# Kernel tuning notes

Measured on AMD Instinct MI355X. Metric: run time of the kernel, lower is better.

The kernel has to match this reference:

```python
import jax, jax.numpy as jnp
import numpy as np

B, S, D, E = 8, 2048, 1024, 8


def setup_inputs() -> dict:
    key = jax.random.key(0)
    k1, k2, k3, k4 = jax.random.split(key, 4)
    return {
        "x": jax.random.normal(k1, (B, S, D), dtype=jnp.float32),
        "routing_scores": jax.random.normal(k2, (B, E), dtype=jnp.float32),
        "expert_w": jax.random.normal(k3, (E, D, D), dtype=jnp.float32) / np.sqrt(D),
        "expert_b": jax.random.normal(k4, (E, D), dtype=jnp.float32),
        "k": 2,
    }


def reference(x, routing_scores, expert_w, expert_b, k):
    batch = routing_scores.shape[0]
    # top-k gating mask + renormalization scale (torch.topk + scatter_ equivalent)
    values, indices = jax.lax.top_k(routing_scores, k)              # (B, k)
    mask = jnp.zeros_like(routing_scores, dtype=bool)
    mask = mask.at[jnp.arange(batch)[:, None], indices].set(True)    # (B, E)
    scale = 1.0 / (values.sum(axis=1, keepdims=True) + 1e-8)         # (B, 1)
    masked_scores = scale * routing_scores * mask                    # (B, E)

    # dense per-expert transform: expert_e(x) = x @ W_e + b_e  -> (E, B, S, D)
    expert_out = jnp.einsum("bsd,edf->ebsf", x, expert_w) + expert_b[:, None, None, :]
    # weighted scatter-accumulate over experts (zero weight for inactive pairs)
    final_output = jnp.einsum("be,ebsf->bsf", masked_scores, expert_out)

    return final_output, mask.sum(axis=0)
```

## Files before the change

### kernel.cpp

```cpp
#include <hip/hip_runtime.h>

#define NB 8
#define NS 2048
#define ND 1024
#define NE 8

typedef unsigned short ushort_t;
typedef __attribute__((ext_vector_type(8))) short bf16x8;
typedef __attribute__((ext_vector_type(4))) float f32x4;

__device__ __forceinline__ unsigned short f2bf(float f) {
    union { float f; unsigned int u; } x; x.f = f;
    unsigned int u = x.u + 0x7fffu + ((x.u >> 16) & 1u);
    return (unsigned short)(u >> 16);
}

__device__ __forceinline__ void gload16(const void* g, void* l) {
    __builtin_amdgcn_global_load_lds(
        (const __attribute__((address_space(1))) unsigned int*)g,
        (__attribute__((address_space(3))) unsigned int*)l, 16, 0, 0);
}

__device__ __forceinline__ void coef_local(const float* __restrict__ scores,
                                           int b, int k, float* cf) {
    float s[NE];
#pragma unroll
    for (int e = 0; e < NE; ++e) s[e] = scores[b * NE + e];
    bool sel[NE];
#pragma unroll
    for (int e = 0; e < NE; ++e) sel[e] = false;
    float sum = 0.f;
    for (int j = 0; j < k; ++j) {
        int best = 0; float bv = -3.4e38f;
#pragma unroll
        for (int e = 0; e < NE; ++e)
            if (!sel[e] && s[e] > bv) { bv = s[e]; best = e; }
        sel[best] = true; sum += bv;
    }
    float scale = 1.f / (sum + 1e-8f);
#pragma unroll
    for (int e = 0; e < NE; ++e) cf[e] = sel[e] ? scale * s[e] : 0.f;
}

__global__ void prep_kernel(const float* __restrict__ x,
                            const float* __restrict__ scores,
                            const float* __restrict__ W,
                            const float* __restrict__ eb,
                            const int* __restrict__ kp,
                            ushort_t* __restrict__ xb,
                            ushort_t* __restrict__ wct,
                            float* __restrict__ bias,
                            float* __restrict__ counts) {
    __shared__ float tile[64][65];
    __shared__ int selS[NB][NE];
    int bid = blockIdx.x;
    int t = threadIdx.x;

    if (bid < 2048) {
        int b = bid >> 8;
        int f0 = (bid & 15) * 64, d0 = ((bid >> 4) & 15) * 64;
        float cf[NE];
        coef_local(scores, b, kp[0], cf);
        int lr = t >> 4;
        int lc = (t & 15) * 4;
        float4 acc[4];
#pragma unroll
        for (int it = 0; it < 4; ++it) acc[it] = make_float4(0.f, 0.f, 0.f, 0.f);
#pragma unroll
        for (int e = 0; e < NE; ++e) {
            float c = cf[e];
            if (c != 0.f) {
                const float* We = W + ((size_t)e * ND * ND);
#pragma unroll
                for (int it = 0; it < 4; ++it) {
                    int d = d0 + lr + it * 16;
                    float4 v = *(const float4*)(We + (size_t)d * ND + f0 + lc);
                    acc[it].x += c * v.x; acc[it].y += c * v.y;
                    acc[it].z += c * v.z; acc[it].w += c * v.w;
                }
            }
        }
#pragma unroll
        for (int it = 0; it < 4; ++it) {
            int r = lr + it * 16;
            tile[r][lc + 0] = acc[it].x; tile[r][lc + 1] = acc[it].y;
            tile[r][lc + 2] = acc[it].z; tile[r][lc + 3] = acc[it].w;
        }
        __syncthreads();
        int dl = t & 63;
        int frow = t >> 6;
        ushort_t* dst = wct + (size_t)b * ND * ND + (size_t)f0 * ND + d0 + dl;
#pragma unroll
        for (int it = 0; it < 16; ++it) {
            int f = frow + it * 4;
            dst[(size_t)f * ND] = f2bf(tile[dl][f]);
        }
    } else if (bid < 10240) {
        size_t i = (size_t)(bid - 2048) * 256 + t;
        const float4* p = (const float4*)x + 2 * i;
        float4 a = p[0], b = p[1];
        uint4 o;
        o.x = (unsigned)f2bf(a.x) | ((unsigned)f2bf(a.y) << 16);
        o.y = (unsigned)f2bf(a.z) | ((unsigned)f2bf(a.w) << 16);
        o.z = (unsigned)f2bf(b.x) | ((unsigned)f2bf(b.y) << 16);
        o.w = (unsigned)f2bf(b.z) | ((unsigned)f2bf(b.w) << 16);
        ((uint4*)xb)[i] = o;
    } else if (bid < 10272) {
        int i = bid - 10240;
        int b = i >> 2, f = (i & 3) * 256 + t;
        float cf[NE];
        coef_local(scores, b, kp[0], cf);
        float acc = 0.f;
#pragma unroll
        for (int e = 0; e < NE; ++e)
            if (cf[e] != 0.f) acc += cf[e] * eb[e * ND + f];
        bias[b * ND + f] = acc;
    } else {
        int k = kp[0];
        if (t < NB) {
            float s[NE];
#pragma unroll
            for (int e = 0; e < NE; ++e) s[e] = scores[t * NE + e];
            bool sel[NE];
#pragma unroll
            for (int e = 0; e < NE; ++e) sel[e] = false;
            for (int j = 0; j < k; ++j) {
                int best = 0; float bv = -3.4e38f;
#pragma unroll
                for (int e = 0; e < NE; ++e)
                    if (!sel[e] && s[e] > bv) { bv = s[e]; best = e; }
                sel[best] = true;
            }
#pragma unroll
            for (int e = 0; e < NE; ++e) selS[t][e] = sel[e] ? 1 : 0;
        }
        __syncthreads();
        if (t < NE) {
            int c = 0;
#pragma unroll
            for (int b = 0; b < NB; ++b) c += selS[b][t];
            counts[t] = (float)c;
        }
    }
}

__global__ __launch_bounds__(512, 2) void gemm_kernel(const ushort_t* __restrict__ xb,
                                                      const ushort_t* __restrict__ wct,
                                                      const float* __restrict__ bias,
                                                      float* __restrict__ out) {
    __shared__ ushort_t ldsA[3][256 * 32];
    __shared__ ushort_t ldsB[3][256 * 32];

    int bid = blockIdx.x;
    int b = bid & 7;
    int tile = bid >> 3;
    int m0 = (tile >> 2) * 256;
    int n0 = (tile & 3) * 256;
    const ushort_t* A  = xb  + ((size_t)b * NS * ND) + (size_t)m0 * ND;
    const ushort_t* Bt = wct + ((size_t)b * ND * ND) + (size_t)n0 * ND;

    int t = threadIdx.x, lane = t & 63, wave = t >> 6;
    int wm = wave >> 2, wn = wave & 3;
    int fr = lane & 15, fq = lane >> 4;

    int swz_s = (lane & 3) ^ ((lane >> 3) & 3);
    const ushort_t* srcA = A  + (size_t)(wave * 16 + (lane >> 2)) * ND + swz_s * 8;
    const ushort_t* srcB = Bt + (size_t)(wave * 16 + (lane >> 2)) * ND + swz_s * 8;
    int dst0 = wave * 512;
    int dst1 = (8 + wave) * 512;

    int swz_r = fq ^ ((fr >> 1) & 3);
    int offA = (wm * 128 + fr) * 32 + swz_r * 8;
    int offB = (wn * 64  + fr) * 32 + swz_r * 8;

    f32x4 acc[8][4];
#pragma unroll
    for (int i = 0; i < 8; ++i)
#pragma unroll
        for (int j = 0; j < 4; ++j) acc[i][j] = (f32x4){0.f, 0.f, 0.f, 0.f};

    const int NT = 32;

#define STAGE(kt, buf) do { \
    gload16(srcA + (kt) * 32,                     &ldsA[buf][dst0]); \
    gload16(srcA + (kt) * 32 + 128 * ND,          &ldsA[buf][dst1]); \
    gload16(srcB + (kt) * 32,                     &ldsB[buf][dst0]); \
    gload16(srcB + (kt) * 32 + 128 * ND,          &ldsB[buf][dst1]); \
} while (0)

#define READF(aR, bR, rb) do { \
    const ushort_t* pA_ = &ldsA[rb][0] + offA; \
    const ushort_t* pB_ = &ldsB[rb][0] + offB; \
    _Pragma("unroll") \
    for (int nj = 0; nj < 4; ++nj) bR[nj] = *(const bf16x8*)(pB_ + nj * 512); \
    _Pragma("unroll") \
    for (int mi = 0; mi < 8; ++mi) aR[mi] = *(const bf16x8*)(pA_ + mi * 512); \
} while (0)

#define MFMA_T(aR, bR) do { \
    __builtin_amdgcn_s_setprio(1); \
    _Pragma("unroll") \
    for (int mi = 0; mi < 8; ++mi) \
        _Pragma("unroll") \
        for (int nj = 0; nj < 4; ++nj) \
            acc[mi][nj] = __builtin_amdgcn_mfma_f32_16x16x32_bf16(aR[mi], bR[nj], acc[mi][nj], 0, 0, 0); \
    __builtin_amdgcn_s_setprio(0); \
} while (0)

#define TILE_END(j) do { \
    if ((j) + 2 < NT) { \
        asm volatile("s_waitcnt lgkmcnt(0)" ::: "memory"); \
        if ((j) + 3 < NT) asm volatile("s_waitcnt vmcnt(4)" ::: "memory"); \
        else              asm volatile("s_waitcnt vmcnt(0)" ::: "memory"); \
        __builtin_amdgcn_s_barrier(); \
    } \
} while (0)

    bf16x8 aX[8], bX[4], aY[8], bY[4];

    STAGE(0, 0); STAGE(1, 1); STAGE(2, 2);
    asm volatile("s_waitcnt vmcnt(4)" ::: "memory");
    __builtin_amdgcn_s_barrier();
    READF(aX, bX, 0);
    asm volatile("s_waitcnt lgkmcnt(0)" ::: "memory");
    __builtin_amdgcn_s_barrier();

    int cs = 0;
    for (int kt = 0; kt < NT; kt += 2) {
        int rb = cs + 1; if (rb == 3) rb = 0;
        READF(aY, bY, rb);
        if (kt + 3 < NT) STAGE(kt + 3, cs);
        __builtin_amdgcn_sched_barrier(0);
        MFMA_T(aX, bX);
        __builtin_amdgcn_sched_barrier(0);
        TILE_END(kt);

        int rb2 = rb + 1; if (rb2 == 3) rb2 = 0;
        if (kt + 2 < NT) READF(aX, bX, rb2);
        if (kt + 4 < NT) STAGE(kt + 4, rb);
        __builtin_amdgcn_sched_barrier(0);
        MFMA_T(aY, bY);
        __builtin_amdgcn_sched_barrier(0);
        TILE_END(kt + 1);

        cs = rb2;
    }

#undef STAGE
#undef READF
#undef MFMA_T
#undef TILE_END

    const float* bs = bias + b * ND;
    float* O = out + ((size_t)b * NS * ND);
#pragma unroll
    for (int mi = 0; mi < 8; ++mi) {
        int row = m0 + wm * 128 + mi * 16 + fq * 4;
#pragma unroll
        for (int nj = 0; nj < 4; ++nj) {
            int col = n0 + wn * 64 + nj * 16 + fr;
            float bv = bs[col];
            f32x4 v = acc[mi][nj];
#pragma unroll
            for (int r = 0; r < 4; ++r)
                O[(size_t)(row + r) * ND + col] = v[r] + bv;
        }
    }
}

extern "C" void kernel_launch(void* const* d_in, const int* in_sizes, int n_in,
                              void* d_out, int out_size, void* d_ws, size_t ws_size,
                              hipStream_t stream) {
    const float* x      = (const float*)d_in[0];
    const float* scores = (const float*)d_in[1];
    const float* Wx     = (const float*)d_in[2];
    const float* eb     = (const float*)d_in[3];
    const int*   kp     = (const int*)d_in[4];
    float* out = (float*)d_out;
    char* ws = (char*)d_ws;

    float*    bias  = (float*)(ws + 1024);
    ushort_t* xbuf  = (ushort_t*)(ws + 65536);
    ushort_t* wct   = (ushort_t*)(ws + 65536 + (size_t)NB * NS * ND * 2);
    float*    counts = out + (size_t)NB * NS * ND;

    prep_kernel<<<10273, 256, 0, stream>>>(x, scores, Wx, eb, kp, xbuf, wct, bias, counts);
    gemm_kernel<<<256, 512, 0, stream>>>(xbuf, wct, bias, out);
}
```

Measured before the change: 67.18 us.

## Restructure GEMM main loop into four-phase ping-pong with finer-grained staging

Replaces the triple-buffered 32-wide K pipeline with a double-buffered 64-wide K tile split into two halves. Each K step becomes four phases of 16 MFMAs, and each phase interleaves a slice of LDS fragment reads and global-to-LDS loads with a barrier gate. The LDS swizzle and per-thread staging layout also change. The aim is to lower register pressure and overlap memory traffic with MFMA work more finely, at the cost of more barriers per K step.

```diff
diff --git a/kernel.cpp b/kernel.cpp
--- a/kernel.cpp
+++ b/kernel.cpp
@@ -148,8 +148,8 @@
                                                       const ushort_t* __restrict__ wct,
                                                       const float* __restrict__ bias,
                                                       float* __restrict__ out) {
-    __shared__ ushort_t ldsA[3][256 * 32];
-    __shared__ ushort_t ldsB[3][256 * 32];
+    __shared__ ushort_t ldsA[2][2][256 * 32];
+    __shared__ ushort_t ldsB[2][2][256 * 32];
 
     int bid = blockIdx.x;
     int b = bid & 7;
@@ -163,15 +163,18 @@
     int wm = wave >> 2, wn = wave & 3;
     int fr = lane & 15, fq = lane >> 4;
 
-    int swz_s = (lane & 3) ^ ((lane >> 3) & 3);
-    const ushort_t* srcA = A  + (size_t)(wave * 16 + (lane >> 2)) * ND + swz_s * 8;
-    const ushort_t* srcB = Bt + (size_t)(wave * 16 + (lane >> 2)) * ND + swz_s * 8;
-    int dst0 = wave * 512;
-    int dst1 = (8 + wave) * 512;
-
-    int swz_r = fq ^ ((fr >> 1) & 3);
-    int offA = (wm * 128 + fr) * 32 + swz_r * 8;
-    int offB = (wn * 64  + fr) * 32 + swz_r * 8;
+    int srow = t >> 2;
+    int slotg = (t & 3) ^ ((srow ^ (srow >> 2)) & 3);
+    const ushort_t* sA = A  + (size_t)srow * ND + slotg * 8;
+    const ushort_t* sB = Bt + (size_t)srow * ND + slotg * 8;
+    int ldst = t * 8;
+
+    int swzb = (fq ^ ((fr ^ (fr >> 2)) & 3)) * 16;
+    int aoff[8], boff[4];
+#pragma unroll
+    for (int mi = 0; mi < 8; ++mi) aoff[mi] = (wm * 128 + mi * 16 + fr) * 64 + swzb;
+#pragma unroll
+    for (int nj = 0; nj < 4; ++nj) boff[nj] = (wn * 64 + nj * 16 + fr) * 64 + swzb;
 
     f32x4 acc[8][4];
 #pragma unroll
@@ -179,77 +182,87 @@
 #pragma unroll
         for (int j = 0; j < 4; ++j) acc[i][j] = (f32x4){0.f, 0.f, 0.f, 0.f};
 
-    const int NT = 32;
-
-#define STAGE(kt, buf) do { \
-    gload16(srcA + (kt) * 32,                     &ldsA[buf][dst0]); \
-    gload16(srcA + (kt) * 32 + 128 * ND,          &ldsA[buf][dst1]); \
-    gload16(srcB + (kt) * 32,                     &ldsB[buf][dst0]); \
-    gload16(srcB + (kt) * 32 + 128 * ND,          &ldsB[buf][dst1]); \
+    const int NT = ND / 64;
+
+#define STG_A(kh, ktt, bf) do { \
+    gload16(sA + (ktt) * 64 + (kh) * 32,            &ldsA[bf][kh][ldst]); \
+    gload16(sA + (ktt) * 64 + (kh) * 32 + 128 * ND, &ldsA[bf][kh][4096 + ldst]); \
 } while (0)
-
-#define READF(aR, bR, rb) do { \
-    const ushort_t* pA_ = &ldsA[rb][0] + offA; \
-    const ushort_t* pB_ = &ldsB[rb][0] + offB; \
-    _Pragma("unroll") \
-    for (int nj = 0; nj < 4; ++nj) bR[nj] = *(const bf16x8*)(pB_ + nj * 512); \
-    _Pragma("unroll") \
-    for (int mi = 0; mi < 8; ++mi) aR[mi] = *(const bf16x8*)(pA_ + mi * 512); \
+#define STG_B(kh, ktt, bf) do { \
+    gload16(sB + (ktt) * 64 + (kh) * 32,            &ldsB[bf][kh][ldst]); \
+    gload16(sB + (ktt) * 64 + (kh) * 32 + 128 * ND, &ldsB[bf][kh][4096 + ldst]); \
 } while (0)
-
-#define MFMA_T(aR, bR) do { \
+#define PH_GATE do { \
+    __builtin_amdgcn_sched_barrier(0); \
+    __builtin_amdgcn_s_barrier(); \
+    asm volatile("s_waitcnt lgkmcnt(0)" ::: "memory"); \
+    __builtin_amdgcn_sched_barrier(0); \
+} while (0)
+#define MFMA16(base, aR, bR) do { \
     __builtin_amdgcn_s_setprio(1); \
     _Pragma("unroll") \
-    for (int mi = 0; mi < 8; ++mi) \
+    for (int mi = 0; mi < 4; ++mi) \
         _Pragma("unroll") \
         for (int nj = 0; nj < 4; ++nj) \
-            acc[mi][nj] = __builtin_amdgcn_mfma_f32_16x16x32_bf16(aR[mi], bR[nj], acc[mi][nj], 0, 0, 0); \
+            acc[(base) + mi][nj] = __builtin_amdgcn_mfma_f32_16x16x32_bf16(aR[mi], bR[nj], acc[(base) + mi][nj], 0, 0, 0); \
     __builtin_amdgcn_s_setprio(0); \
+    __builtin_amdgcn_sched_barrier(0); \
 } while (0)
 
-#define TILE_END(j) do { \
-    if ((j) + 2 < NT) { \
-        asm volatile("s_waitcnt lgkmcnt(0)" ::: "memory"); \
-        if ((j) + 3 < NT) asm volatile("s_waitcnt vmcnt(4)" ::: "memory"); \
-        else              asm volatile("s_waitcnt vmcnt(0)" ::: "memory"); \
-        __builtin_amdgcn_s_barrier(); \
-    } \
-} while (0)
-
-    bf16x8 aX[8], bX[4], aY[8], bY[4];
-
-    STAGE(0, 0); STAGE(1, 1); STAGE(2, 2);
-    asm volatile("s_waitcnt vmcnt(4)" ::: "memory");
+    STG_A(0, 0, 0); STG_B(0, 0, 0); STG_A(1, 0, 0); STG_B(1, 0, 0);
+    STG_A(0, 1, 1); STG_B(0, 1, 1);
+    asm volatile("s_waitcnt vmcnt(8)" ::: "memory");
     __builtin_amdgcn_s_barrier();
-    READF(aX, bX, 0);
-    asm volatile("s_waitcnt lgkmcnt(0)" ::: "memory");
-    __builtin_amdgcn_s_barrier();
-
-    int cs = 0;
-    for (int kt = 0; kt < NT; kt += 2) {
-        int rb = cs + 1; if (rb == 3) rb = 0;
-        READF(aY, bY, rb);
-        if (kt + 3 < NT) STAGE(kt + 3, cs);
-        __builtin_amdgcn_sched_barrier(0);
-        MFMA_T(aX, bX);
-        __builtin_amdgcn_sched_barrier(0);
-        TILE_END(kt);
-
-        int rb2 = rb + 1; if (rb2 == 3) rb2 = 0;
-        if (kt + 2 < NT) READF(aX, bX, rb2);
-        if (kt + 4 < NT) STAGE(kt + 4, rb);
-        __builtin_amdgcn_sched_barrier(0);
-        MFMA_T(aY, bY);
-        __builtin_amdgcn_sched_barrier(0);
-        TILE_END(kt + 1);
-
-        cs = rb2;
+
+    for (int kt = 0; kt < NT; ++kt) {
+        int buf = kt & 1, nb = buf ^ 1;
+        const char* lA0 = (const char*)&ldsA[buf][0][0];
+        const char* lA1 = (const char*)&ldsA[buf][1][0];
+        const char* lB0 = (const char*)&ldsB[buf][0][0];
+        const char* lB1 = (const char*)&ldsB[buf][1][0];
+        bf16x8 aX[4], aY[4], bX[4], bY[4];
+
+#pragma unroll
+        for (int nj = 0; nj < 4; ++nj) bX[nj] = *(const bf16x8*)(lB0 + boff[nj]);
+#pragma unroll
+        for (int mi = 0; mi < 4; ++mi) aX[mi] = *(const bf16x8*)(lA0 + aoff[mi]);
+        if (kt + 1 < NT) STG_A(1, kt + 1, nb);
+        PH_GATE;
+        MFMA16(0, aX, bX);
+        __builtin_amdgcn_s_barrier();
+
+#pragma unroll
+        for (int mi = 0; mi < 4; ++mi) aY[mi] = *(const bf16x8*)(lA0 + aoff[mi + 4]);
+        if (kt + 1 < NT) STG_B(1, kt + 1, nb);
+        PH_GATE;
+        MFMA16(4, aY, bX);
+        if (kt < NT - 1) asm volatile("s_waitcnt vmcnt(8)" ::: "memory");
+        else             asm volatile("s_waitcnt vmcnt(0)" ::: "memory");
+        __builtin_amdgcn_s_barrier();
+
+#pragma unroll
+        for (int nj = 0; nj < 4; ++nj) bY[nj] = *(const bf16x8*)(lB1 + boff[nj]);
+#pragma unroll
+        for (int mi = 0; mi < 4; ++mi) aX[mi] = *(const bf16x8*)(lA1 + aoff[mi]);
+        if (kt + 2 < NT) STG_A(0, kt + 2, buf);
+        PH_GATE;
+        MFMA16(0, aX, bY);
+        __builtin_amdgcn_s_barrier();
+
+#pragma unroll
+        for (int mi = 0; mi < 4; ++mi) aY[mi] = *(const bf16x8*)(lA1 + aoff[mi + 4]);
+        if (kt + 2 < NT) STG_B(0, kt + 2, buf);
+        PH_GATE;
+        MFMA16(4, aY, bY);
+        if (kt < NT - 2)       asm volatile("s_waitcnt vmcnt(8)" ::: "memory");
+        else if (kt == NT - 2) asm volatile("s_waitcnt vmcnt(4)" ::: "memory");
+        if (kt < NT - 1) __builtin_amdgcn_s_barrier();
     }
 
-#undef STAGE
-#undef READF
-#undef MFMA_T
-#undef TILE_END
+#undef STG_A
+#undef STG_B
+#undef PH_GATE
+#undef MFMA16
 
     const float* bs = bias + b * ND;
     float* O = out + ((size_t)b * NS * ND);
```

After: 71.47 us. 1.06x slower.

## Shrink GEMM tile to 256x128 with single-buffered register pipeline and more blocks

Applied to the files above, without the earlier changes.

Halves the N tile from 256 to 128, so the grid doubles to 512 blocks and each wave holds a 4x4 accumulator array instead of 8x4. Launch bounds are raised to allow four blocks per CU. The double register-buffered fragment pipeline is replaced by a simpler per-k-step loop that loads fragments, waits on LDS, and issues the MFMAs, with a three-stage LDS ring prefetching two tiles ahead. The aim is better occupancy and CU balance across 256 CUs, at the cost of lower arithmetic intensity per tile and less overlap between LDS reads and MFMAs.

```diff
diff --git a/kernel.cpp b/kernel.cpp
--- a/kernel.cpp
+++ b/kernel.cpp
@@ -144,118 +144,97 @@
     }
 }
 
-__global__ __launch_bounds__(512, 2) void gemm_kernel(const ushort_t* __restrict__ xb,
+__global__ __launch_bounds__(512, 4) void gemm_kernel(const ushort_t* __restrict__ xb,
                                                       const ushort_t* __restrict__ wct,
                                                       const float* __restrict__ bias,
                                                       float* __restrict__ out) {
     __shared__ ushort_t ldsA[3][256 * 32];
-    __shared__ ushort_t ldsB[3][256 * 32];
+    __shared__ ushort_t ldsB[3][128 * 32];
 
     int bid = blockIdx.x;
     int b = bid & 7;
     int tile = bid >> 3;
-    int m0 = (tile >> 2) * 256;
-    int n0 = (tile & 3) * 256;
+    int m0 = (tile >> 3) * 256;
+    int n0 = (tile & 7) * 128;
     const ushort_t* A  = xb  + ((size_t)b * NS * ND) + (size_t)m0 * ND;
     const ushort_t* Bt = wct + ((size_t)b * ND * ND) + (size_t)n0 * ND;
 
     int t = threadIdx.x, lane = t & 63, wave = t >> 6;
-    int wm = wave >> 2, wn = wave & 3;
+    int wm = wave >> 1, wn = wave & 1;
     int fr = lane & 15, fq = lane >> 4;
 
-    int swz_s = (lane & 3) ^ ((lane >> 3) & 3);
-    const ushort_t* srcA = A  + (size_t)(wave * 16 + (lane >> 2)) * ND + swz_s * 8;
-    const ushort_t* srcB = Bt + (size_t)(wave * 16 + (lane >> 2)) * ND + swz_s * 8;
-    int dst0 = wave * 512;
-    int dst1 = (8 + wave) * 512;
-
-    int swz_r = fq ^ ((fr >> 1) & 3);
-    int offA = (wm * 128 + fr) * 32 + swz_r * 8;
-    int offB = (wn * 64  + fr) * 32 + swz_r * 8;
-
-    f32x4 acc[8][4];
-#pragma unroll
-    for (int i = 0; i < 8; ++i)
+    int srow = t >> 2;
+    int slotg = (t & 3) ^ ((srow >> 1) & 3);
+    const ushort_t* sA = A  + (size_t)srow * ND + slotg * 8;
+    const ushort_t* sB = Bt + (size_t)srow * ND + slotg * 8;
+    int ldst = t * 8;
+
+    int swzb = (fq ^ ((fr >> 1) & 3)) * 16;
+    int aoff[4], boff[4];
+#pragma unroll
+    for (int mi = 0; mi < 4; ++mi) aoff[mi] = (wm * 64 + mi * 16 + fr) * 64 + swzb;
+#pragma unroll
+    for (int nj = 0; nj < 4; ++nj) boff[nj] = (wn * 64 + nj * 16 + fr) * 64 + swzb;
+
+    f32x4 acc[4][4];
+#pragma unroll
+    for (int i = 0; i < 4; ++i)
 #pragma unroll
         for (int j = 0; j < 4; ++j) acc[i][j] = (f32x4){0.f, 0.f, 0.f, 0.f};
 
-    const int NT = 32;
+    const int NT = ND / 32;
 
 #define STAGE(kt, buf) do { \
-    gload16(srcA + (kt) * 32,                     &ldsA[buf][dst0]); \
-    gload16(srcA + (kt) * 32 + 128 * ND,          &ldsA[buf][dst1]); \
-    gload16(srcB + (kt) * 32,                     &ldsB[buf][dst0]); \
-    gload16(srcB + (kt) * 32 + 128 * ND,          &ldsB[buf][dst1]); \
+    gload16(sA + (kt) * 32,            &ldsA[buf][ldst]); \
+    gload16(sA + (kt) * 32 + 128 * ND, &ldsA[buf][4096 + ldst]); \
+    gload16(sB + (kt) * 32,            &ldsB[buf][ldst]); \
 } while (0)
 
-#define READF(aR, bR, rb) do { \
-    const ushort_t* pA_ = &ldsA[rb][0] + offA; \
-    const ushort_t* pB_ = &ldsB[rb][0] + offB; \
-    _Pragma("unroll") \
-    for (int nj = 0; nj < 4; ++nj) bR[nj] = *(const bf16x8*)(pB_ + nj * 512); \
-    _Pragma("unroll") \
-    for (int mi = 0; mi < 8; ++mi) aR[mi] = *(const bf16x8*)(pA_ + mi * 512); \
-} while (0)
-
-#define MFMA_T(aR, bR) do { \
-    __builtin_amdgcn_s_setprio(1); \
-    _Pragma("unroll") \
-    for (int mi = 0; mi < 8; ++mi) \
-        _Pragma("unroll") \
-        for (int nj = 0; nj < 4; ++nj) \
-            acc[mi][nj] = __builtin_amdgcn_mfma_f32_16x16x32_bf16(aR[mi], bR[nj], acc[mi][nj], 0, 0, 0); \
-    __builtin_amdgcn_s_setprio(0); \
-} while (0)
-
-#define TILE_END(j) do { \
-    if ((j) + 2 < NT) { \
-        asm volatile("s_waitcnt lgkmcnt(0)" ::: "memory"); \
-        if ((j) + 3 < NT) asm volatile("s_waitcnt vmcnt(4)" ::: "memory"); \
-        else              asm volatile("s_waitcnt vmcnt(0)" ::: "memory"); \
-        __builtin_amdgcn_s_barrier(); \
-    } \
-} while (0)
-
-    bf16x8 aX[8], bX[4], aY[8], bY[4];
-
-    STAGE(0, 0); STAGE(1, 1); STAGE(2, 2);
-    asm volatile("s_waitcnt vmcnt(4)" ::: "memory");
+    STAGE(0, 0);
+    STAGE(1, 1);
+    asm volatile("s_waitcnt vmcnt(3)" ::: "memory");
     __builtin_amdgcn_s_barrier();
-    READF(aX, bX, 0);
-    asm volatile("s_waitcnt lgkmcnt(0)" ::: "memory");
-    __builtin_amdgcn_s_barrier();
-
-    int cs = 0;
-    for (int kt = 0; kt < NT; kt += 2) {
-        int rb = cs + 1; if (rb == 3) rb = 0;
-        READF(aY, bY, rb);
-        if (kt + 3 < NT) STAGE(kt + 3, cs);
-        __builtin_amdgcn_sched_barrier(0);
-        MFMA_T(aX, bX);
-        __builtin_amdgcn_sched_barrier(0);
-        TILE_END(kt);
-
-        int rb2 = rb + 1; if (rb2 == 3) rb2 = 0;
-        if (kt + 2 < NT) READF(aX, bX, rb2);
-        if (kt + 4 < NT) STAGE(kt + 4, rb);
-        __builtin_amdgcn_sched_barrier(0);
-        MFMA_T(aY, bY);
-        __builtin_amdgcn_sched_barrier(0);
-        TILE_END(kt + 1);
-
-        cs = rb2;
+
+    int cur = 0;
+    for (int kt = 0; kt < NT; ++kt) {
+        const char* lA = (const char*)&ldsA[cur][0];
+        const char* lB = (const char*)&ldsB[cur][0];
+        int sq = cur + 2; if (sq >= 3) sq -= 3;
+
+        __builtin_amdgcn_sched_barrier(0);
+        bf16x8 af[4], bf[4];
+#pragma unroll
+        for (int nj = 0; nj < 4; ++nj) bf[nj] = *(const bf16x8*)(lB + boff[nj]);
+#pragma unroll
+        for (int mi = 0; mi < 4; ++mi) af[mi] = *(const bf16x8*)(lA + aoff[mi]);
+        if (kt + 2 < NT) STAGE(kt + 2, sq);
+        __builtin_amdgcn_sched_barrier(0);
+        asm volatile("s_waitcnt lgkmcnt(0)" ::: "memory");
+        __builtin_amdgcn_sched_barrier(0);
+        __builtin_amdgcn_s_setprio(1);
+#pragma unroll
+        for (int mi = 0; mi < 4; ++mi)
+#pragma unroll
+            for (int nj = 0; nj < 4; ++nj)
+                acc[mi][nj] = __builtin_amdgcn_mfma_f32_16x16x32_bf16(af[mi], bf[nj], acc[mi][nj], 0, 0, 0);
+        __builtin_amdgcn_s_setprio(0);
+        __builtin_amdgcn_sched_barrier(0);
+        if (kt + 2 < NT) {
+            asm volatile("s_waitcnt vmcnt(3)" ::: "memory");
+        } else if (kt + 1 < NT) {
+            asm volatile("s_waitcnt vmcnt(0)" ::: "memory");
+        }
+        if (kt + 1 < NT) __builtin_amdgcn_s_barrier();
+        cur += 1; if (cur == 3) cur = 0;
     }
 
 #undef STAGE
-#undef READF
-#undef MFMA_T
-#undef TILE_END
 
     const float* bs = bias + b * ND;
     float* O = out + ((size_t)b * NS * ND);
 #pragma unroll
-    for (int mi = 0; mi < 8; ++mi) {
-        int row = m0 + wm * 128 + mi * 16 + fq * 4;
+    for (int mi = 0; mi < 4; ++mi) {
+        int row = m0 + wm * 64 + mi * 16 + fq * 4;
 #pragma unroll
         for (int nj = 0; nj < 4; ++nj) {
             int col = n0 + wn * 64 + nj * 16 + fr;
@@ -285,5 +264,5 @@
     float*    counts = out + (size_t)NB * NS * ND;
 
     prep_kernel<<<10273, 256, 0, stream>>>(x, scores, Wx, eb, kp, xbuf, wct, bias, counts);
-    gemm_kernel<<<256, 512, 0, stream>>>(xbuf, wct, bias, out);
-}
+    gemm_kernel<<<512, 512, 0, stream>>>(xbuf, wct, bias, out);
+}
```

Result: no change. 67.53 us (+0.5%).
